# Kernel optimization log

Hardware: AMD Instinct MI355X
Metric: run time of the kernel (lower is better)

The kernel has to match this reference:

```python
import jax, jax.numpy as jnp
import numpy as np

EPS_R = 1e-6


def setup_inputs() -> dict:
    key = jax.random.key(0)
    k1, k2, k3 = jax.random.split(key, 3)
    N, F, C = 32768, 2048, 64
    X = jax.random.normal(k1, (N, F), dtype=jnp.float32)
    W = jax.random.normal(k2, (C, F), dtype=jnp.float32) * 0.1  # matches init std=0.1
    r = jax.random.uniform(k3, (F,), dtype=jnp.float32)
    return {"X": X, "W": W, "r": r}


def reference(X, W, r):
    # Weighted squared distances: d[n, c] = sum_f r_f * (X[n,f] - W[c,f])**2
    # Expanded form avoids the [N, C, F] intermediate:
    #   d = (X^2) @ r + (W^2) @ r - 2 * X @ (r * W)^T
    rc = jnp.clip(r, EPS_R, None)
    x_sq = (X * X) @ rc                      # [N]
    w_sq = (W * W) @ rc                      # [C]
    cross = X @ (W * rc).T                   # [N, C]  (dominant GEMM)
    dists = x_sq[:, None] + w_sq[None, :] - 2.0 * cross  # [N, C]
    # One prototype per class with label = class index, per init_prototypes.
    preds = jnp.argmin(dists, axis=1)        # [N] int
    return dists, preds
```

## Files before the change

### kernel.cpp

```cpp
#include <hip/hip_runtime.h>

#define NROWS 32768
#define FDIM  2048
#define CDIM  64
#define BM    64
#define BK    32
#define NCH   (FDIM / BK)
#define SA    40
#define EPS_R 1e-6f
#define WSCALE 1024.0f
#define DESCALE (2.0f / WSCALE)

typedef __attribute__((ext_vector_type(8))) _Float16 half8;
typedef __attribute__((ext_vector_type(4))) float    f32x4;

__device__ __forceinline__ unsigned packh(_Float16 a, _Float16 b) {
    return (unsigned)__builtin_bit_cast(unsigned short, a) |
           ((unsigned)__builtin_bit_cast(unsigned short, b) << 16);
}

__device__ __forceinline__ void split2(float a, float b, unsigned& hi, unsigned& lo) {
    _Float16 ha = (_Float16)a, hb = (_Float16)b;
    _Float16 la = (_Float16)(a - (float)ha), lb = (_Float16)(b - (float)hb);
    hi = packh(ha, hb);
    lo = packh(la, lb);
}

__global__ __launch_bounds__(256) void gmlvq_prep(
    const float* __restrict__ W, const float* __restrict__ r,
    unsigned short* __restrict__ Bh, unsigned short* __restrict__ Bl,
    float* __restrict__ wsq, float* __restrict__ rc_out) {
    const int c = blockIdx.x;
    const int tid = threadIdx.x;
    const int f0 = tid * 8;

    const float* Wp = W + (size_t)c * FDIM + f0;
    float4 w0 = *(const float4*)Wp;
    float4 w1 = *(const float4*)(Wp + 4);
    float4 r0 = *(const float4*)(r + f0);
    float4 r1 = *(const float4*)(r + f0 + 4);
    r0.x = fmaxf(r0.x, EPS_R); r0.y = fmaxf(r0.y, EPS_R);
    r0.z = fmaxf(r0.z, EPS_R); r0.w = fmaxf(r0.w, EPS_R);
    r1.x = fmaxf(r1.x, EPS_R); r1.y = fmaxf(r1.y, EPS_R);
    r1.z = fmaxf(r1.z, EPS_R); r1.w = fmaxf(r1.w, EPS_R);

    if (c == 0) {
        *(float4*)(rc_out + f0) = r0;
        *(float4*)(rc_out + f0 + 4) = r1;
    }

    float rw0 = r0.x * w0.x, rw1 = r0.y * w0.y, rw2 = r0.z * w0.z, rw3 = r0.w * w0.w;
    float rw4 = r1.x * w1.x, rw5 = r1.y * w1.y, rw6 = r1.z * w1.z, rw7 = r1.w * w1.w;

    float part = rw0 * w0.x + rw1 * w0.y + rw2 * w0.z + rw3 * w0.w
               + rw4 * w1.x + rw5 * w1.y + rw6 * w1.z + rw7 * w1.w;

    unsigned h01, l01, h23, l23, h45, l45, h67, l67;
    split2(rw0 * WSCALE, rw1 * WSCALE, h01, l01);
    split2(rw2 * WSCALE, rw3 * WSCALE, h23, l23);
    split2(rw4 * WSCALE, rw5 * WSCALE, h45, l45);
    split2(rw6 * WSCALE, rw7 * WSCALE, h67, l67);

    *(uint4*)(Bh + (size_t)c * FDIM + f0) = make_uint4(h01, h23, h45, h67);
    *(uint4*)(Bl + (size_t)c * FDIM + f0) = make_uint4(l01, l23, l45, l67);

#pragma unroll
    for (int m = 32; m; m >>= 1) part += __shfl_xor(part, m);
    __shared__ float red[4];
    if ((tid & 63) == 0) red[tid >> 6] = part;
    __syncthreads();
    if (tid == 0) wsq[c] = (red[0] + red[1]) + (red[2] + red[3]);
}

__global__ __launch_bounds__(256, 3) void gmlvq_main(
    const float* __restrict__ X, const float* __restrict__ rc,
    const unsigned short* __restrict__ Bh, const unsigned short* __restrict__ Bl,
    const float* __restrict__ wsq_g,
    float* __restrict__ dists, float* __restrict__ preds) {

    __shared__ __align__(16) unsigned short lds_bh[2][CDIM * SA];
    __shared__ __align__(16) unsigned short lds_bl[2][CDIM * SA];
    __shared__ float lds_xsq[BM];
    __shared__ float lds_wsq[CDIM];

    const int tid  = threadIdx.x;
    const int wave = tid >> 6;
    const int lane = tid & 63;
    const int quad = lane >> 4;
    const int l15  = lane & 15;
    const int row_base = blockIdx.x * BM;
    const int cB   = tid >> 2;
    const int segB = (tid & 3) * 8;

    if (tid < CDIM) lds_wsq[tid] = wsq_g[tid];

    const float* Ap = X + (size_t)(row_base + wave * 16 + l15) * FDIM + quad * 8;
    const float* Rp = rc + quad * 8;
    const unsigned short* Bhp = Bh + (size_t)cB * FDIM + segB;
    const unsigned short* Blp = Bl + (size_t)cB * FDIM + segB;

    uint4 b0h = *(const uint4*)(Bhp);
    uint4 b0l = *(const uint4*)(Blp);
    *(uint4*)&lds_bh[0][cB * SA + segB] = b0h;
    *(uint4*)&lds_bl[0][cB * SA + segB] = b0l;
    uint4 bnh = *(const uint4*)(Bhp + BK);
    uint4 bnl = *(const uint4*)(Blp + BK);

    float4 a0 = *(const float4*)(Ap);
    float4 a1 = *(const float4*)(Ap + 4);
    float4 r0 = *(const float4*)(Rp);
    float4 r1 = *(const float4*)(Rp + 4);

    float p = 0.f;
    f32x4 acc[4];
#pragma unroll
    for (int n = 0; n < 4; n++) acc[n] = (f32x4){0.f, 0.f, 0.f, 0.f};

#pragma unroll 2
    for (int c = 0; c < NCH; c++) {
        __syncthreads();

        const int kn = ((c + 1) & (NCH - 1)) * BK;
        const int kf = ((c + 2) & (NCH - 1)) * BK;
        const float4 a0n = *(const float4*)(Ap + kn);
        const float4 a1n = *(const float4*)(Ap + kn + 4);
        const float4 r0n = *(const float4*)(Rp + kn);
        const float4 r1n = *(const float4*)(Rp + kn + 4);
        const uint4  bfh = *(const uint4*)(Bhp + kf);
        const uint4  bfl = *(const uint4*)(Blp + kf);

        half8 ah, al;
        {
            const float va[8] = {a0.x, a0.y, a0.z, a0.w, a1.x, a1.y, a1.z, a1.w};
            const float vr[8] = {r0.x, r0.y, r0.z, r0.w, r1.x, r1.y, r1.z, r1.w};
#pragma unroll
            for (int j = 0; j < 8; j++) {
                const float v = va[j];
                const _Float16 h = (_Float16)v;
                ah[j] = h;
                al[j] = (_Float16)(v - (float)h);
                p += vr[j] * v * v;
            }
        }

        const int bb = c & 1;
#pragma unroll
        for (int n = 0; n < 4; n++) {
            const half8 bhf = *(const half8*)&lds_bh[bb][(n * 16 + l15) * SA + quad * 8];
            const half8 blf = *(const half8*)&lds_bl[bb][(n * 16 + l15) * SA + quad * 8];
            acc[n] = __builtin_amdgcn_mfma_f32_16x16x32_f16(ah, bhf, acc[n], 0, 0, 0);
            acc[n] = __builtin_amdgcn_mfma_f32_16x16x32_f16(ah, blf, acc[n], 0, 0, 0);
            acc[n] = __builtin_amdgcn_mfma_f32_16x16x32_f16(al, bhf, acc[n], 0, 0, 0);
        }

        *(uint4*)&lds_bh[bb ^ 1][cB * SA + segB] = bnh;
        *(uint4*)&lds_bl[bb ^ 1][cB * SA + segB] = bnl;

        bnh = bfh; bnl = bfl;
        a0 = a0n; a1 = a1n; r0 = r0n; r1 = r1n;
    }

    p += __shfl_xor(p, 16);
    p += __shfl_xor(p, 32);
    if (quad == 0) lds_xsq[wave * 16 + l15] = p;
    __syncthreads();

    float dd[4][4];
#pragma unroll
    for (int n = 0; n < 4; n++) {
#pragma unroll
        for (int rr = 0; rr < 4; rr++) {
            const int m = wave * 16 + quad * 4 + rr;
            const int cc = n * 16 + l15;
            const float d = lds_xsq[m] + lds_wsq[cc] - acc[n][rr] * DESCALE;
            dd[n][rr] = d;
            dists[(size_t)(row_base + m) * CDIM + cc] = d;
        }
    }

#pragma unroll
    for (int rr = 0; rr < 4; rr++) {
        float bv = dd[0][rr];
        int   bi = l15;
#pragma unroll
        for (int n = 1; n < 4; n++) {
            const float v = dd[n][rr];
            const int  ci = n * 16 + l15;
            if (v < bv || (v == bv && ci < bi)) { bv = v; bi = ci; }
        }
#pragma unroll
        for (int mask = 1; mask < 16; mask <<= 1) {
            const float ov = __shfl_xor(bv, mask);
            const int   oi = __shfl_xor(bi, mask);
            if (ov < bv || (ov == bv && oi < bi)) { bv = ov; bi = oi; }
        }
        if (l15 == 0) {
            const int m = wave * 16 + quad * 4 + rr;
            preds[row_base + m] = (float)bi;
        }
    }
}

extern "C" void kernel_launch(void* const* d_in, const int* in_sizes, int n_in,
                              void* d_out, int out_size, void* d_ws, size_t ws_size,
                              hipStream_t stream) {
    const float* X = (const float*)d_in[0];
    const float* W = (const float*)d_in[1];
    const float* r = (const float*)d_in[2];
    float* dists = (float*)d_out;
    float* preds = dists + (size_t)NROWS * CDIM;

    unsigned short* Bh = (unsigned short*)d_ws;
    unsigned short* Bl = Bh + (size_t)CDIM * FDIM;
    float* wsq   = (float*)(Bl + (size_t)CDIM * FDIM);
    float* rc_ws = wsq + CDIM;

    gmlvq_prep<<<dim3(CDIM), dim3(256), 0, stream>>>(W, r, Bh, Bl, wsq, rc_ws);
    gmlvq_main<<<dim3(NROWS / BM), dim3(256), 0, stream>>>(X, rc_ws, Bh, Bl, wsq, dists, preds);
}
```

Before: 389.2 us.

## Load B fragments directly from global into registers, dropping LDS staging and barriers

Each wave now loads its hi/lo B fragments straight from global memory (L2/L1 cached) into registers, prefetching one chunk ahead, instead of staging them through double-buffered shared memory. This removes the per-iteration __syncthreads and the LDS writes and reads. In exchange every wave re-fetches the full B tile (4x redundant global/L1 traffic per block), register pressure rises, and the occupancy hint drops from 3 to 2 blocks per CU.

```diff
diff --git a/kernel.cpp b/kernel.cpp
--- a/kernel.cpp
+++ b/kernel.cpp
@@ -6,7 +6,6 @@
 #define BM    64
 #define BK    32
 #define NCH   (FDIM / BK)
-#define SA    40
 #define EPS_R 1e-6f
 #define WSCALE 1024.0f
 #define DESCALE (2.0f / WSCALE)
@@ -72,14 +71,12 @@
     if (tid == 0) wsq[c] = (red[0] + red[1]) + (red[2] + red[3]);
 }
 
-__global__ __launch_bounds__(256, 3) void gmlvq_main(
+__global__ __launch_bounds__(256, 2) void gmlvq_main(
     const float* __restrict__ X, const float* __restrict__ rc,
     const unsigned short* __restrict__ Bh, const unsigned short* __restrict__ Bl,
     const float* __restrict__ wsq_g,
     float* __restrict__ dists, float* __restrict__ preds) {
 
-    __shared__ __align__(16) unsigned short lds_bh[2][CDIM * SA];
-    __shared__ __align__(16) unsigned short lds_bl[2][CDIM * SA];
     __shared__ float lds_xsq[BM];
     __shared__ float lds_wsq[CDIM];
 
@@ -89,27 +86,25 @@
     const int quad = lane >> 4;
     const int l15  = lane & 15;
     const int row_base = blockIdx.x * BM;
-    const int cB   = tid >> 2;
-    const int segB = (tid & 3) * 8;
 
     if (tid < CDIM) lds_wsq[tid] = wsq_g[tid];
 
     const float* Ap = X + (size_t)(row_base + wave * 16 + l15) * FDIM + quad * 8;
     const float* Rp = rc + quad * 8;
-    const unsigned short* Bhp = Bh + (size_t)cB * FDIM + segB;
-    const unsigned short* Blp = Bl + (size_t)cB * FDIM + segB;
-
-    uint4 b0h = *(const uint4*)(Bhp);
-    uint4 b0l = *(const uint4*)(Blp);
-    *(uint4*)&lds_bh[0][cB * SA + segB] = b0h;
-    *(uint4*)&lds_bl[0][cB * SA + segB] = b0l;
-    uint4 bnh = *(const uint4*)(Bhp + BK);
-    uint4 bnl = *(const uint4*)(Blp + BK);
+    const unsigned short* Bhp = Bh + (size_t)l15 * FDIM + quad * 8;
+    const unsigned short* Blp = Bl + (size_t)l15 * FDIM + quad * 8;
+    const size_t nstride = (size_t)16 * FDIM;
 
     float4 a0 = *(const float4*)(Ap);
     float4 a1 = *(const float4*)(Ap + 4);
     float4 r0 = *(const float4*)(Rp);
     float4 r1 = *(const float4*)(Rp + 4);
+    uint4 bh[4], bl[4];
+#pragma unroll
+    for (int n = 0; n < 4; n++) {
+        bh[n] = *(const uint4*)(Bhp + n * nstride);
+        bl[n] = *(const uint4*)(Blp + n * nstride);
+    }
 
     float p = 0.f;
     f32x4 acc[4];
@@ -118,16 +113,17 @@
 
 #pragma unroll 2
     for (int c = 0; c < NCH; c++) {
-        __syncthreads();
-
         const int kn = ((c + 1) & (NCH - 1)) * BK;
-        const int kf = ((c + 2) & (NCH - 1)) * BK;
         const float4 a0n = *(const float4*)(Ap + kn);
         const float4 a1n = *(const float4*)(Ap + kn + 4);
         const float4 r0n = *(const float4*)(Rp + kn);
         const float4 r1n = *(const float4*)(Rp + kn + 4);
-        const uint4  bfh = *(const uint4*)(Bhp + kf);
-        const uint4  bfl = *(const uint4*)(Blp + kf);
+        uint4 bhn[4], bln[4];
+#pragma unroll
+        for (int n = 0; n < 4; n++) {
+            bhn[n] = *(const uint4*)(Bhp + n * nstride + kn);
+            bln[n] = *(const uint4*)(Blp + n * nstride + kn);
+        }
 
         half8 ah, al;
         {
@@ -143,21 +139,18 @@
             }
         }
 
-        const int bb = c & 1;
 #pragma unroll
         for (int n = 0; n < 4; n++) {
-            const half8 bhf = *(const half8*)&lds_bh[bb][(n * 16 + l15) * SA + quad * 8];
-            const half8 blf = *(const half8*)&lds_bl[bb][(n * 16 + l15) * SA + quad * 8];
+            const half8 bhf = __builtin_bit_cast(half8, bh[n]);
+            const half8 blf = __builtin_bit_cast(half8, bl[n]);
             acc[n] = __builtin_amdgcn_mfma_f32_16x16x32_f16(ah, bhf, acc[n], 0, 0, 0);
             acc[n] = __builtin_amdgcn_mfma_f32_16x16x32_f16(ah, blf, acc[n], 0, 0, 0);
             acc[n] = __builtin_amdgcn_mfma_f32_16x16x32_f16(al, bhf, acc[n], 0, 0, 0);
         }
 
-        *(uint4*)&lds_bh[bb ^ 1][cB * SA + segB] = bnh;
-        *(uint4*)&lds_bl[bb ^ 1][cB * SA + segB] = bnl;
-
-        bnh = bfh; bnl = bfl;
         a0 = a0n; a1 = a1n; r0 = r0n; r1 = r1n;
+#pragma unroll
+        for (int n = 0; n < 4; n++) { bh[n] = bhn[n]; bl[n] = bln[n]; }
     }
 
     p += __shfl_xor(p, 16);
```

Measured after the change: 455.2 us. 1.17x slower.
